# Kernel optimization log

Hardware: AMD Instinct MI355X
Metric: run time of the kernel (lower is better)

## Reference

```python
import jax, jax.numpy as jnp
import numpy as np

N_NODES = 50000
N_EDGES = 800000
D_FEAT = 64


def setup_inputs() -> dict:
    key = jax.random.key(0)
    k1, k2, k3 = jax.random.split(key, 3)
    x_sum = jax.random.normal(k1, (N_NODES, D_FEAT), dtype=jnp.float32)
    x_prod = jax.random.uniform(k2, (N_NODES, D_FEAT), dtype=jnp.float32)
    edge_index = jax.random.randint(k3, (2, N_EDGES), 0, N_NODES, dtype=jnp.int64)
    return {"x_sum": x_sum, "x_prod": x_prod, "edge_index": edge_index}


def reference(x_sum, x_prod, edge_index):
    # flow='source_to_target' -> gather from edge_index[0], aggregate at edge_index[1]
    src_idx = edge_index[0]
    dst_idx = edge_index[1]
    n = x_sum.shape[0]

    # __lift__: index_select along node dim (message is identity; edge_attr/norm None)
    m_sum = x_sum[src_idx]    # [E, D]
    m_prod = x_prod[src_idx]  # [E, D]

    # scatter_sum: zeros-init + scatter_add_
    out_sum = jax.ops.segment_sum(m_sum, dst_idx, num_segments=n)

    # scatter_product: ones-init + scatter_(reduce='multiply')
    out_prod = jnp.ones((n, x_prod.shape[1]), dtype=x_prod.dtype).at[dst_idx].multiply(m_prod)

    return out_sum, out_prod
```

## Files before the change

### kernel.cpp

```cpp
#include <hip/hip_runtime.h>
#include <hip/hip_fp16.h>

#define N_NODES 50000
#define N_EDGES 800000
#define D_FEAT  64
#define BSHIFT  6
#define NBKT    782
#define NB      256
#define CHUNK   3125
#define PSHIFT  20
#define SRC_MASK ((1 << PSHIFT) - 1)
#define CAP     6144

#define WS_TOT    0
#define WS_BH     784
#define WS_PAIR   (WS_BH + NBKT * NB)
#define WS_SSRC   (WS_PAIR + N_EDGES)
#define WS_PACKED (WS_SSRC + N_EDGES)
#define WS_INTS   (WS_PACKED + N_NODES * D_FEAT)

__device__ inline void detect_idx_layout(const int* idx, int* flag) {
    int allzero = 1;
    #pragma unroll
    for (int i = 1; i < 129; i += 2) {
        if (idx[i] != 0) allzero = 0;
    }
    *flag = allzero;
}

__global__ __launch_bounds__(256) void cast_hist(int* __restrict__ W,
                                                 const int* __restrict__ idx,
                                                 const float* __restrict__ xs,
                                                 const float* __restrict__ xp) {
    __shared__ int h[NBKT];
    __shared__ int flg_s;
    const int t = threadIdx.x;
    for (int i = t; i < NBKT; i += 256) h[i] = 0;
    if (t == 0) detect_idx_layout(idx, &flg_s);
    __syncthreads();

    const float4* xs4 = (const float4*)xs;
    const float4* xp4 = (const float4*)xp;
    uint4* pk4 = (uint4*)(W + WS_PACKED);
    union { __half2 h2; unsigned int u; } c0, c1, c2, c3;
    const int tid = blockIdx.x * 256 + t;
    for (int g = tid; g < (N_NODES * D_FEAT) / 4; g += NB * 256) {
        float4 a = xs4[g], b = xp4[g];
        c0.h2 = __floats2half2_rn(a.x, b.x);
        c1.h2 = __floats2half2_rn(a.y, b.y);
        c2.h2 = __floats2half2_rn(a.z, b.z);
        c3.h2 = __floats2half2_rn(a.w, b.w);
        pk4[g] = make_uint4(c0.u, c1.u, c2.u, c3.u);
    }

    const int flg = flg_s;
    const int base = blockIdx.x * CHUNK;
    for (int e = base + t; e < base + CHUNK; e += 256) {
        int dst = flg ? idx[2 * (N_EDGES + e)] : idx[N_EDGES + e];
        atomicAdd(&h[dst >> BSHIFT], 1);
    }
    __syncthreads();
    for (int i = t; i < NBKT; i += 256)
        W[WS_BH + i * NB + blockIdx.x] = h[i];
}

__global__ __launch_bounds__(256) void bucket_scan(int* __restrict__ W) {
    __shared__ int part[NB];
    int j = blockIdx.x;
    int t = threadIdx.x;
    int c = W[WS_BH + j * NB + t];
    part[t] = c;
    __syncthreads();
    for (int off = 1; off < NB; off <<= 1) {
        int u = (t >= off) ? part[t - off] : 0;
        __syncthreads();
        part[t] += u;
        __syncthreads();
    }
    W[WS_BH + j * NB + t] = part[t] - c;
    if (t == NB - 1) W[WS_TOT + j] = part[t];
}

__global__ __launch_bounds__(256) void coarse_scatter(const int* __restrict__ idx,
                                                      int* __restrict__ W) {
    __shared__ int cur[NBKT];
    __shared__ int flg_s;
    const int t = threadIdx.x;
    for (int i = t; i < NBKT; i += 256) cur[i] = W[WS_TOT + i];
    if (t == 0) detect_idx_layout(idx, &flg_s);
    __syncthreads();
    if (t < 64) {
        int vals[13];
        int sum = 0;
        const int base = t * 13;
        #pragma unroll
        for (int j = 0; j < 13; ++j) {
            int k = base + j;
            vals[j] = (k < NBKT) ? cur[k] : 0;
            sum += vals[j];
        }
        int incl = sum;
        #pragma unroll
        for (int off = 1; off < 64; off <<= 1) {
            int u = __shfl_up(incl, off, 64);
            if (t >= off) incl += u;
        }
        int run = incl - sum;
        #pragma unroll
        for (int j = 0; j < 13; ++j) {
            int k = base + j;
            if (k < NBKT) cur[k] = run;
            run += vals[j];
        }
    }
    __syncthreads();
    for (int i = t; i < NBKT; i += 256) cur[i] += W[WS_BH + i * NB + blockIdx.x];
    __syncthreads();
    const int flg = flg_s;
    const int base = blockIdx.x * CHUNK;
    for (int e = base + t; e < base + CHUNK; e += 256) {
        int src, dst;
        if (flg) { src = idx[2 * e]; dst = idx[2 * (N_EDGES + e)]; }
        else     { src = idx[e];     dst = idx[N_EDGES + e]; }
        int pos = atomicAdd(&cur[dst >> BSHIFT], 1);
        W[WS_PAIR + pos] = src | ((dst & 63) << PSHIFT);
    }
}

__global__ __launch_bounds__(512) void sort_gather(int* __restrict__ W,
                                                   float* __restrict__ out) {
    __shared__ int ssrc_l[CAP];
    __shared__ int red[512];
    __shared__ int h[64];
    __shared__ int noff[65];
    const int b = blockIdx.x;
    const int t = threadIdx.x;

    int part = 0;
    for (int k = t; k < b; k += 512) part += W[WS_TOT + k];
    red[t] = part;
    if (t < 64) h[t] = 0;
    __syncthreads();
    #pragma unroll
    for (int off = 256; off > 0; off >>= 1) {
        if (t < off) red[t] += red[t + off];
        __syncthreads();
    }
    const int bbase = red[0];
    const int bend  = bbase + W[WS_TOT + b];
    const int nedge = bend - bbase;

    for (int e = bbase + t; e < bend; e += 512)
        atomicAdd(&h[(unsigned)W[WS_PAIR + e] >> PSHIFT], 1);
    __syncthreads();
    if (t < 64) {
        int c = h[t];
        int incl = c;
        #pragma unroll
        for (int off = 1; off < 64; off <<= 1) {
            int u = __shfl_up(incl, off, 64);
            if (t >= off) incl += u;
        }
        noff[t] = incl - c;
        if (t == 63) noff[64] = incl;
        h[t] = incl - c;
    }
    __syncthreads();

    const bool fits = (nedge <= CAP);
    if (fits) {
        for (int e = bbase + t; e < bend; e += 512) {
            int v = W[WS_PAIR + e];
            int p = atomicAdd(&h[(unsigned)v >> PSHIFT], 1);
            ssrc_l[p] = v & SRC_MASK;
        }
    } else {
        for (int e = bbase + t; e < bend; e += 512) {
            int v = W[WS_PAIR + e];
            int p = atomicAdd(&h[(unsigned)v >> PSHIFT], 1);
            W[WS_SSRC + bbase + p] = v & SRC_MASK;
        }
    }
    __syncthreads();

    const __half2* packed = (const __half2*)(W + WS_PACKED);
    const int wave = t >> 6;
    const int lane = t & 63;
    for (int nn = wave; nn < 64; nn += 8) {
        const int node = (b << BSHIFT) + nn;
        if (node >= N_NODES) break;
        int beg = __builtin_amdgcn_readfirstlane(noff[nn]);
        int end = __builtin_amdgcn_readfirstlane(noff[nn + 1]);

        float s0 = 0.f, s1 = 0.f, s2 = 0.f, s3 = 0.f;
        float s4 = 0.f, s5 = 0.f, s6 = 0.f, s7 = 0.f;
        float p0 = 1.f, p1 = 1.f, p2 = 1.f, p3 = 1.f;
        float p4 = 1.f, p5 = 1.f, p6 = 1.f, p7 = 1.f;
        if (fits) {
            int i = beg;
            for (; i + 7 < end; i += 8) {
                int a0 = ssrc_l[i],     a1 = ssrc_l[i + 1];
                int a2 = ssrc_l[i + 2], a3 = ssrc_l[i + 3];
                int a4 = ssrc_l[i + 4], a5 = ssrc_l[i + 5];
                int a6 = ssrc_l[i + 6], a7 = ssrc_l[i + 7];
                float2 f0 = __half22float2(packed[a0 * D_FEAT + lane]);
                float2 f1 = __half22float2(packed[a1 * D_FEAT + lane]);
                float2 f2 = __half22float2(packed[a2 * D_FEAT + lane]);
                float2 f3 = __half22float2(packed[a3 * D_FEAT + lane]);
                float2 f4 = __half22float2(packed[a4 * D_FEAT + lane]);
                float2 f5 = __half22float2(packed[a5 * D_FEAT + lane]);
                float2 f6 = __half22float2(packed[a6 * D_FEAT + lane]);
                float2 f7 = __half22float2(packed[a7 * D_FEAT + lane]);
                s0 += f0.x; s1 += f1.x; s2 += f2.x; s3 += f3.x;
                s4 += f4.x; s5 += f5.x; s6 += f6.x; s7 += f7.x;
                p0 *= f0.y; p1 *= f1.y; p2 *= f2.y; p3 *= f3.y;
                p4 *= f4.y; p5 *= f5.y; p6 *= f6.y; p7 *= f7.y;
            }
            for (; i + 1 < end; i += 2) {
                int a0 = ssrc_l[i], a1 = ssrc_l[i + 1];
                float2 f0 = __half22float2(packed[a0 * D_FEAT + lane]);
                float2 f1 = __half22float2(packed[a1 * D_FEAT + lane]);
                s0 += f0.x; s1 += f1.x;
                p0 *= f0.y; p1 *= f1.y;
            }
            if (i < end) {
                float2 f = __half22float2(packed[ssrc_l[i] * D_FEAT + lane]);
                s0 += f.x;
                p0 *= f.y;
            }
        } else {
            for (int i = beg; i < end; ++i) {
                int a = W[WS_SSRC + bbase + i];
                float2 f = __half22float2(packed[a * D_FEAT + lane]);
                s0 += f.x;
                p0 *= f.y;
            }
        }
        float ssum = ((s0 + s1) + (s2 + s3)) + ((s4 + s5) + (s6 + s7));
        float pprd = ((p0 * p1) * (p2 * p3)) * ((p4 * p5) * (p6 * p7));
        out[(long)node * D_FEAT + lane] = ssum;
        out[(long)N_NODES * D_FEAT + (long)node * D_FEAT + lane] = pprd;
    }
}

__device__ inline void atomicMulF32(float* addr, float val) {
    unsigned int* ua = (unsigned int*)addr;
    unsigned int old = __hip_atomic_load(ua, __ATOMIC_RELAXED, __HIP_MEMORY_SCOPE_AGENT);
    while (true) {
        unsigned int assumed = old;
        unsigned int desired = __float_as_uint(__uint_as_float(assumed) * val);
        old = atomicCAS(ua, assumed, desired);
        if (old == assumed) break;
    }
}

__global__ void fb_init(float* __restrict__ out, int* __restrict__ flag,
                        const int* __restrict__ idx) {
    const int n4 = (N_NODES * D_FEAT) / 4;
    int tid = blockIdx.x * blockDim.x + threadIdx.x;
    int stride = gridDim.x * blockDim.x;
    float4* o = (float4*)out;
    const float4 z = make_float4(0.f, 0.f, 0.f, 0.f);
    const float4 one = make_float4(1.f, 1.f, 1.f, 1.f);
    for (int i = tid; i < n4; i += stride) { o[i] = z; o[n4 + i] = one; }
    if (blockIdx.x == 0 && threadIdx.x == 0) detect_idx_layout(idx, flag);
}

__global__ void fb_scatter(const float* __restrict__ xs, const float* __restrict__ xp,
                           const int* __restrict__ idx, float* __restrict__ out,
                           const int* __restrict__ flag) {
    long tid = (long)blockIdx.x * blockDim.x + threadIdx.x;
    const long total = (long)N_EDGES * (D_FEAT / 4);
    if (tid >= total) return;
    int e = (int)(tid >> 4);
    int c = (int)(tid & 15);
    int src, dst;
    if (*flag) { src = idx[2 * e]; dst = idx[2 * (N_EDGES + e)]; }
    else       { src = idx[e];     dst = idx[N_EDGES + e]; }
    const float4 s = ((const float4*)(xs + (long)src * D_FEAT))[c];
    const float4 p = ((const float4*)(xp + (long)src * D_FEAT))[c];
    float* os = out + (long)dst * D_FEAT + c * 4;
    float* op = out + (long)N_NODES * D_FEAT + (long)dst * D_FEAT + c * 4;
    atomicAdd(os + 0, s.x); atomicAdd(os + 1, s.y);
    atomicAdd(os + 2, s.z); atomicAdd(os + 3, s.w);
    atomicMulF32(op + 0, p.x); atomicMulF32(op + 1, p.y);
    atomicMulF32(op + 2, p.z); atomicMulF32(op + 3, p.w);
}

extern "C" void kernel_launch(void* const* d_in, const int* in_sizes, int n_in,
                              void* d_out, int out_size, void* d_ws, size_t ws_size,
                              hipStream_t stream) {
    const float* x_sum  = (const float*)d_in[0];
    const float* x_prod = (const float*)d_in[1];
    const int*   eidx   = (const int*)d_in[2];
    float* out = (float*)d_out;
    int* W = (int*)d_ws;

    if (ws_size < (size_t)WS_INTS * sizeof(int)) {
        fb_init<<<1024, 256, 0, stream>>>(out, W, eidx);
        const long total = (long)N_EDGES * (D_FEAT / 4);
        int grid = (int)((total + 255) / 256);
        fb_scatter<<<grid, 256, 0, stream>>>(x_sum, x_prod, eidx, out, W);
        return;
    }

    cast_hist<<<NB, 256, 0, stream>>>(W, eidx, x_sum, x_prod);
    bucket_scan<<<NBKT, 256, 0, stream>>>(W);
    coarse_scatter<<<NB, 256, 0, stream>>>(eidx, W);
    sort_gather<<<NBKT, 512, 0, stream>>>(W, out);
}
```

Baseline: 142.3 us.

## Fuse four-kernel bucket sort pipeline into one cooperative kernel with grid syncs

```diff
diff --git a/kernel.cpp b/kernel.cpp
--- a/kernel.cpp
+++ b/kernel.cpp
@@ -1,16 +1,24 @@
 #include <hip/hip_runtime.h>
 #include <hip/hip_fp16.h>
+#include <hip/hip_cooperative_groups.h>
+
+namespace cg = cooperative_groups;
 
 #define N_NODES 50000
 #define N_EDGES 800000
 #define D_FEAT  64
 #define BSHIFT  6
 #define NBKT    782
-#define NB      256
-#define CHUNK   3125
 #define PSHIFT  20
 #define SRC_MASK ((1 << PSHIFT) - 1)
 #define CAP     6144
+
+#define CNB     391
+#define CTH     512
+#define CCHUNK  2047
+
+#define NB      256
+#define CHUNK   3125
 
 #define WS_TOT    0
 #define WS_BH     784
@@ -26,6 +34,229 @@
         if (idx[i] != 0) allzero = 0;
     }
     *flag = allzero;
+}
+
+__global__ __launch_bounds__(1024) void zero_gcur(int* __restrict__ W) {
+    int t = threadIdx.x;
+    if (t < NBKT) W[WS_TOT + t] = 0;
+}
+
+__global__ __launch_bounds__(CTH, 4) void mega(int* __restrict__ W,
+                                               const int* __restrict__ idx,
+                                               const float* __restrict__ xs,
+                                               const float* __restrict__ xp,
+                                               float* __restrict__ out) {
+    cg::grid_group gg = cg::this_grid();
+    __shared__ int hcur[NBKT];
+    __shared__ int coff[NBKT + 1];
+    __shared__ int pair_l[CAP];
+    __shared__ int ssrc_l[CAP];
+    __shared__ int h64[64];
+    __shared__ int noff[65];
+    __shared__ int flg_s;
+
+    const int t = threadIdx.x;
+    const int b = blockIdx.x;
+
+    for (int i = t; i < NBKT; i += CTH) hcur[i] = 0;
+    if (t == 0) detect_idx_layout(idx, &flg_s);
+    __syncthreads();
+    const int flg = flg_s;
+
+    {
+        const float4* xs4 = (const float4*)xs;
+        const float4* xp4 = (const float4*)xp;
+        uint4* pk4 = (uint4*)(W + WS_PACKED);
+        union { __half2 h2; unsigned int u; } c0, c1, c2, c3;
+        const int gtid = b * CTH + t;
+        for (int g = gtid; g < (N_NODES * D_FEAT) / 4; g += CNB * CTH) {
+            float4 a = xs4[g], p = xp4[g];
+            c0.h2 = __floats2half2_rn(a.x, p.x);
+            c1.h2 = __floats2half2_rn(a.y, p.y);
+            c2.h2 = __floats2half2_rn(a.z, p.z);
+            c3.h2 = __floats2half2_rn(a.w, p.w);
+            pk4[g] = make_uint4(c0.u, c1.u, c2.u, c3.u);
+        }
+    }
+
+    const int ebase = b * CCHUNK;
+    const int eend  = min(ebase + CCHUNK, N_EDGES);
+    int src_r[4], dst_r[4];
+    #pragma unroll
+    for (int i = 0; i < 4; ++i) {
+        int e = ebase + t + i * CTH;
+        bool v = (e < eend);
+        int s = 0, d = 0;
+        if (v) {
+            if (flg) {
+                int2 sp = ((const int2*)idx)[e];
+                int2 dp = ((const int2*)idx)[N_EDGES + e];
+                s = sp.x; d = dp.x;
+            } else {
+                s = idx[e]; d = idx[N_EDGES + e];
+            }
+            atomicAdd(&hcur[d >> BSHIFT], 1);
+        }
+        src_r[i] = v ? s : -1;
+        dst_r[i] = d;
+    }
+    __syncthreads();
+
+    for (int j = t; j < NBKT; j += CTH) {
+        int c = hcur[j];
+        hcur[j] = (c > 0) ? atomicAdd(&W[WS_TOT + j], c) : 0;
+    }
+
+    gg.sync();
+
+    for (int j = t; j < NBKT; j += CTH) coff[j] = W[WS_TOT + j];
+    __syncthreads();
+    if (t < 64) {
+        int vals[13];
+        int sum = 0;
+        const int base = t * 13;
+        #pragma unroll
+        for (int j2 = 0; j2 < 13; ++j2) {
+            int k = base + j2;
+            vals[j2] = (k < NBKT) ? coff[k] : 0;
+            sum += vals[j2];
+        }
+        int incl = sum;
+        #pragma unroll
+        for (int off = 1; off < 64; off <<= 1) {
+            int u = __shfl_up(incl, off, 64);
+            if (t >= off) incl += u;
+        }
+        int run = incl - sum;
+        #pragma unroll
+        for (int j2 = 0; j2 < 13; ++j2) {
+            int k = base + j2;
+            if (k < NBKT) coff[k] = run;
+            run += vals[j2];
+        }
+    }
+    if (t == 0) coff[NBKT] = N_EDGES;
+    __syncthreads();
+    for (int j = t; j < NBKT; j += CTH) hcur[j] += coff[j];
+    __syncthreads();
+
+    #pragma unroll
+    for (int i = 0; i < 4; ++i) {
+        if (src_r[i] >= 0) {
+            int d = dst_r[i];
+            int pos = atomicAdd(&hcur[d >> BSHIFT], 1);
+            W[WS_PAIR + pos] = src_r[i] | ((d & 63) << PSHIFT);
+        }
+    }
+
+    gg.sync();
+
+    const __half2* packed = (const __half2*)(W + WS_PACKED);
+    const int wave = t >> 6;
+    const int lane = t & 63;
+    for (int bk = 2 * b; bk < 2 * b + 2; ++bk) {
+        const int bbase = coff[bk];
+        const int bend  = coff[bk + 1];
+        const int nedge = bend - bbase;
+        const bool fits = (nedge <= CAP);
+        if (t < 64) h64[t] = 0;
+        __syncthreads();
+        if (fits) {
+            for (int e = t; e < nedge; e += CTH) {
+                int v = W[WS_PAIR + bbase + e];
+                pair_l[e] = v;
+                atomicAdd(&h64[(unsigned)v >> PSHIFT], 1);
+            }
+        } else {
+            for (int e = t; e < nedge; e += CTH)
+                atomicAdd(&h64[(unsigned)W[WS_PAIR + bbase + e] >> PSHIFT], 1);
+        }
+        __syncthreads();
+        if (t < 64) {
+            int c = h64[t];
+            int incl = c;
+            #pragma unroll
+            for (int off = 1; off < 64; off <<= 1) {
+                int u = __shfl_up(incl, off, 64);
+                if (t >= off) incl += u;
+            }
+            noff[t] = incl - c;
+            if (t == 63) noff[64] = incl;
+            h64[t] = incl - c;
+        }
+        __syncthreads();
+        if (fits) {
+            for (int e = t; e < nedge; e += CTH) {
+                int v = pair_l[e];
+                int p = atomicAdd(&h64[(unsigned)v >> PSHIFT], 1);
+                ssrc_l[p] = v & SRC_MASK;
+            }
+        } else {
+            for (int e = t; e < nedge; e += CTH) {
+                int v = W[WS_PAIR + bbase + e];
+                int p = atomicAdd(&h64[(unsigned)v >> PSHIFT], 1);
+                W[WS_SSRC + bbase + p] = v & SRC_MASK;
+            }
+        }
+        __syncthreads();
+
+        for (int nn = wave; nn < 64; nn += 8) {
+            const int node = (bk << BSHIFT) + nn;
+            if (node >= N_NODES) break;
+            int beg = __builtin_amdgcn_readfirstlane(noff[nn]);
+            int end = __builtin_amdgcn_readfirstlane(noff[nn + 1]);
+
+            float s0 = 0.f, s1 = 0.f, s2 = 0.f, s3 = 0.f;
+            float s4 = 0.f, s5 = 0.f, s6 = 0.f, s7 = 0.f;
+            float p0 = 1.f, p1 = 1.f, p2 = 1.f, p3 = 1.f;
+            float p4 = 1.f, p5 = 1.f, p6 = 1.f, p7 = 1.f;
+            if (fits) {
+                int i = beg;
+                for (; i + 7 < end; i += 8) {
+                    int a0 = ssrc_l[i],     a1 = ssrc_l[i + 1];
+                    int a2 = ssrc_l[i + 2], a3 = ssrc_l[i + 3];
+                    int a4 = ssrc_l[i + 4], a5 = ssrc_l[i + 5];
+                    int a6 = ssrc_l[i + 6], a7 = ssrc_l[i + 7];
+                    float2 f0 = __half22float2(packed[a0 * D_FEAT + lane]);
+                    float2 f1 = __half22float2(packed[a1 * D_FEAT + lane]);
+                    float2 f2 = __half22float2(packed[a2 * D_FEAT + lane]);
+                    float2 f3 = __half22float2(packed[a3 * D_FEAT + lane]);
+                    float2 f4 = __half22float2(packed[a4 * D_FEAT + lane]);
+                    float2 f5 = __half22float2(packed[a5 * D_FEAT + lane]);
+                    float2 f6 = __half22float2(packed[a6 * D_FEAT + lane]);
+                    float2 f7 = __half22float2(packed[a7 * D_FEAT + lane]);
+                    s0 += f0.x; s1 += f1.x; s2 += f2.x; s3 += f3.x;
+                    s4 += f4.x; s5 += f5.x; s6 += f6.x; s7 += f7.x;
+                    p0 *= f0.y; p1 *= f1.y; p2 *= f2.y; p3 *= f3.y;
+                    p4 *= f4.y; p5 *= f5.y; p6 *= f6.y; p7 *= f7.y;
+                }
+                for (; i + 1 < end; i += 2) {
+                    int a0 = ssrc_l[i], a1 = ssrc_l[i + 1];
+                    float2 f0 = __half22float2(packed[a0 * D_FEAT + lane]);
+                    float2 f1 = __half22float2(packed[a1 * D_FEAT + lane]);
+                    s0 += f0.x; s1 += f1.x;
+                    p0 *= f0.y; p1 *= f1.y;
+                }
+                if (i < end) {
+                    float2 f = __half22float2(packed[ssrc_l[i] * D_FEAT + lane]);
+                    s0 += f.x;
+                    p0 *= f.y;
+                }
+            } else {
+                for (int i = beg; i < end; ++i) {
+                    int a = W[WS_SSRC + bbase + i];
+                    float2 f = __half22float2(packed[a * D_FEAT + lane]);
+                    s0 += f.x;
+                    p0 *= f.y;
+                }
+            }
+            float ssum = ((s0 + s1) + (s2 + s3)) + ((s4 + s5) + (s6 + s7));
+            float pprd = ((p0 * p1) * (p2 * p3)) * ((p4 * p5) * (p6 * p7));
+            out[(long)node * D_FEAT + lane] = ssum;
+            out[(long)N_NODES * D_FEAT + (long)node * D_FEAT + lane] = pprd;
+        }
+        __syncthreads();
+    }
 }
 
 __global__ __launch_bounds__(256) void cast_hist(int* __restrict__ W,
@@ -38,21 +269,19 @@
     for (int i = t; i < NBKT; i += 256) h[i] = 0;
     if (t == 0) detect_idx_layout(idx, &flg_s);
     __syncthreads();
-
     const float4* xs4 = (const float4*)xs;
     const float4* xp4 = (const float4*)xp;
     uint4* pk4 = (uint4*)(W + WS_PACKED);
     union { __half2 h2; unsigned int u; } c0, c1, c2, c3;
     const int tid = blockIdx.x * 256 + t;
     for (int g = tid; g < (N_NODES * D_FEAT) / 4; g += NB * 256) {
-        float4 a = xs4[g], b = xp4[g];
-        c0.h2 = __floats2half2_rn(a.x, b.x);
-        c1.h2 = __floats2half2_rn(a.y, b.y);
-        c2.h2 = __floats2half2_rn(a.z, b.z);
-        c3.h2 = __floats2half2_rn(a.w, b.w);
+        float4 a = xs4[g], p = xp4[g];
+        c0.h2 = __floats2half2_rn(a.x, p.x);
+        c1.h2 = __floats2half2_rn(a.y, p.y);
+        c2.h2 = __floats2half2_rn(a.z, p.z);
+        c3.h2 = __floats2half2_rn(a.w, p.w);
         pk4[g] = make_uint4(c0.u, c1.u, c2.u, c3.u);
     }
-
     const int flg = flg_s;
     const int base = blockIdx.x * CHUNK;
     for (int e = base + t; e < base + CHUNK; e += 256) {
@@ -135,7 +364,6 @@
     __shared__ int noff[65];
     const int b = blockIdx.x;
     const int t = threadIdx.x;
-
     int part = 0;
     for (int k = t; k < b; k += 512) part += W[WS_TOT + k];
     red[t] = part;
@@ -149,7 +377,6 @@
     const int bbase = red[0];
     const int bend  = bbase + W[WS_TOT + b];
     const int nedge = bend - bbase;
-
     for (int e = bbase + t; e < bend; e += 512)
         atomicAdd(&h[(unsigned)W[WS_PAIR + e] >> PSHIFT], 1);
     __syncthreads();
@@ -166,7 +393,6 @@
         h[t] = incl - c;
     }
     __syncthreads();
-
     const bool fits = (nedge <= CAP);
     if (fits) {
         for (int e = bbase + t; e < bend; e += 512) {
@@ -182,7 +408,6 @@
         }
     }
     __syncthreads();
-
     const __half2* packed = (const __half2*)(W + WS_PACKED);
     const int wave = t >> 6;
     const int lane = t & 63;
@@ -191,7 +416,6 @@
         if (node >= N_NODES) break;
         int beg = __builtin_amdgcn_readfirstlane(noff[nn]);
         int end = __builtin_amdgcn_readfirstlane(noff[nn + 1]);
-
         float s0 = 0.f, s1 = 0.f, s2 = 0.f, s3 = 0.f;
         float s4 = 0.f, s5 = 0.f, s6 = 0.f, s7 = 0.f;
         float p0 = 1.f, p1 = 1.f, p2 = 1.f, p3 = 1.f;
@@ -304,8 +528,14 @@
         return;
     }
 
-    cast_hist<<<NB, 256, 0, stream>>>(W, eidx, x_sum, x_prod);
-    bucket_scan<<<NBKT, 256, 0, stream>>>(W);
-    coarse_scatter<<<NB, 256, 0, stream>>>(eidx, W);
-    sort_gather<<<NBKT, 512, 0, stream>>>(W, out);
-}
+    zero_gcur<<<1, 1024, 0, stream>>>(W);
+    void* args[] = {(void*)&W, (void*)&eidx, (void*)&x_sum, (void*)&x_prod, (void*)&out};
+    hipError_t err = hipLaunchCooperativeKernel((const void*)mega, dim3(CNB), dim3(CTH),
+                                                args, 0, stream);
+    if (err != hipSuccess) {
+        cast_hist<<<NB, 256, 0, stream>>>(W, eidx, x_sum, x_prod);
+        bucket_scan<<<NBKT, 256, 0, stream>>>(W);
+        coarse_scatter<<<NB, 256, 0, stream>>>(eidx, W);
+        sort_gather<<<NBKT, 512, 0, stream>>>(W, out);
+    }
+}
```

Measured after the change: 239.2 us. +68.0%, slower.
